# Optimization experiments

Hardware: AMD Instinct MI355X
Metric: run time of the kernel (lower is better)

The kernel has to match this reference:

```python
import jax, jax.numpy as jnp
import numpy as np

B, S, NC_CAND = 64, 200, 16
V, NCAT, D, NH, L = 100000, 1000, 256, 8, 2
EU, TKU = 4, 2   # user-block MoE uses EfficientMoELayer defaults
EI, TKI = 8, 2   # item MoE uses config num_experts/top_k
NE_CFG = 8       # load_balance_loss uniform always uses config.num_experts
HID = 2 * D

FLOAT_NAMES = ['item_emb', 'cat_emb', 'ub_in_w', 'ub_in_b', 'ub_out_w', 'ub_out_b',
               'ub_n1_s', 'ub_n1_b', 'ub_n2_s', 'ub_n2_b', 'ub_gate_w', 'ub_gate_b',
               'ub_e_w1', 'ub_e_b1', 'ub_e_w2', 'ub_e_b2', 'un_s', 'un_b',
               'im_gate_w', 'im_gate_b', 'im_e_w1', 'im_e_b1', 'im_e_w2', 'im_e_b2',
               'in_s', 'in_b', 'ca_in_w', 'ca_in_b', 'ca_out_w', 'ca_out_b',
               'fm_w1', 'fm_b1', 'fm_w2', 'fm_b2']


def _ln(x, s, b):
    m = jnp.mean(x, axis=-1, keepdims=True)
    v = jnp.mean((x - m) ** 2, axis=-1, keepdims=True)
    return (x - m) * jax.lax.rsqrt(v + 1e-5) * s + b


def _rope(x):
    # NOTE: faithful to the source's (unconventional) RoPE: x*cos + roll(x,-1)*sin
    s, d = x.shape[1], x.shape[2]
    inv = 1.0 / (10000.0 ** (jnp.arange(0, d, 2, dtype=jnp.float32) / d))
    f = jnp.arange(s, dtype=jnp.float32)[:, None] * inv[None, :]
    emb = jnp.concatenate([f, f], axis=-1)                      # [S, D]
    return x * jnp.cos(emb)[None] + jnp.roll(x, -1, axis=-1) * jnp.sin(emb)[None]


def _self_attn(x, wi, bi, wo, bo):
    b, s, d = x.shape
    hd = d // NH
    q, k, v = jnp.split(x @ wi.T + bi, 3, axis=-1)
    q = q.reshape(b, s, NH, hd)
    k = k.reshape(b, s, NH, hd)
    v = v.reshape(b, s, NH, hd)
    att = jax.nn.softmax(jnp.einsum('bqhd,bkhd->bhqk', q, k) * (hd ** -0.5), axis=-1)
    o = jnp.einsum('bhqk,bkhd->bqhd', att, v).reshape(b, s, d)
    return o @ wo.T + bo


def _moe(xf, gw, gb, w1, b1, w2, b2, top_k):
    # dense-expert compute + sparse top-k combine (same math as masked scatter loop)
    logits = xf @ gw.T + gb                                     # [T, E]
    w = jax.nn.softmax(logits.astype(jnp.float32), axis=-1)
    tw, ti = jax.lax.top_k(w, top_k)
    tw = tw / jnp.sum(tw, axis=-1, keepdims=True)
    e = gw.shape[0]
    cw = jnp.sum(jax.nn.one_hot(ti, e, dtype=tw.dtype) * tw[..., None], axis=1)  # [T, E]
    h = jax.nn.gelu(jnp.einsum('td,ehd->teh', xf, w1) + b1[None], approximate=False)
    y = jnp.einsum('teh,edh->ted', h, w2) + b2[None]
    return jnp.einsum('te,ted->td', cw.astype(xf.dtype), y), logits


def _forward(history_seq, candidate_ids, category_ids, p):
    x = _rope(p['item_emb'][history_seq])                       # [B, S, D]
    routers = []
    for l in range(L):
        a = _self_attn(x, p['ub_in_w'][l], p['ub_in_b'][l], p['ub_out_w'][l], p['ub_out_b'][l])
        x = _ln(x + a, p['ub_n1_s'][l], p['ub_n1_b'][l])
        mo, r = _moe(x.reshape(-1, D), p['ub_gate_w'][l], p['ub_gate_b'][l],
                     p['ub_e_w1'][l], p['ub_e_b1'][l], p['ub_e_w2'][l], p['ub_e_b2'][l], TKU)
        routers.append(r)
        x = _ln(x + mo.reshape(x.shape), p['ub_n2_s'][l], p['ub_n2_b'][l])
    hist = _ln(x, p['un_s'], p['un_b'])                          # [B, S, D]

    ie = p['item_emb'][candidate_ids] + p['cat_emb'][category_ids]  # [B, Nc, D]
    mo_i, r_i = _moe(ie.reshape(-1, D), p['im_gate_w'], p['im_gate_b'],
                     p['im_e_w1'], p['im_e_b1'], p['im_e_w2'], p['im_e_b2'], TKI)
    item = _ln(mo_i.reshape(ie.shape), p['in_s'], p['in_b'])     # [B, Nc, D]

    # cross attention: candidates as length-1 queries over history (no [B*Nc,S,D] expand)
    hd = D // NH
    wq, wk, wv = jnp.split(p['ca_in_w'], 3, axis=0)
    bq, bk, bv = jnp.split(p['ca_in_b'], 3, axis=0)
    q = (item @ wq.T + bq).reshape(B, NC_CAND, NH, hd)
    k = (hist @ wk.T + bk).reshape(B, S, NH, hd)
    v = (hist @ wv.T + bv).reshape(B, S, NH, hd)
    att = jax.nn.softmax(jnp.einsum('bnhd,bshd->bnhs', q, k) * (hd ** -0.5), axis=-1)
    o = jnp.einsum('bnhs,bshd->bnhd', att, v).reshape(B, NC_CAND, D)
    taw = o @ p['ca_out_w'].T + p['ca_out_b']                    # [B, Nc, D]

    fused = jnp.concatenate([taw, item], axis=-1)                # [B, Nc, 2D]
    h = jax.nn.gelu(fused @ p['fm_w1'].T + p['fm_b1'], approximate=False)
    logits = (h @ p['fm_w2'].T + p['fm_b2'])[..., 0]             # [B, Nc]

    aux = jnp.float32(0.0)
    for r in routers + [r_i]:
        avg = jnp.mean(jax.nn.softmax(r, axis=-1), axis=0)
        aux = aux + jnp.mean((avg - 1.0 / NE_CFG) ** 2)
    return logits, aux


def setup_inputs() -> dict:
    key = jax.random.key(0)
    ks = iter(jax.random.split(key, 64))

    def nrm(shape, scale=0.02):
        return jax.random.normal(next(ks), shape, jnp.float32) * scale

    inp = {
        'history_seq': jax.random.randint(next(ks), (B, S), 0, V),
        'candidate_ids': jax.random.randint(next(ks), (B, NC_CAND), 0, V),
        'category_ids': jax.random.randint(next(ks), (B, NC_CAND), 0, NCAT),
        'item_emb': nrm((V, D)), 'cat_emb': nrm((NCAT, D)),
        'ub_in_w': nrm((L, 3 * D, D)), 'ub_in_b': jnp.zeros((L, 3 * D), jnp.float32),
        'ub_out_w': nrm((L, D, D)), 'ub_out_b': jnp.zeros((L, D), jnp.float32),
        'ub_n1_s': jnp.ones((L, D), jnp.float32), 'ub_n1_b': jnp.zeros((L, D), jnp.float32),
        'ub_n2_s': jnp.ones((L, D), jnp.float32), 'ub_n2_b': jnp.zeros((L, D), jnp.float32),
        'ub_gate_w': nrm((L, EU, D)), 'ub_gate_b': jnp.zeros((L, EU), jnp.float32),
        'ub_e_w1': nrm((L, EU, HID, D)), 'ub_e_b1': jnp.zeros((L, EU, HID), jnp.float32),
        'ub_e_w2': nrm((L, EU, D, HID)), 'ub_e_b2': jnp.zeros((L, EU, D), jnp.float32),
        'un_s': jnp.ones((D,), jnp.float32), 'un_b': jnp.zeros((D,), jnp.float32),
        'im_gate_w': nrm((EI, D)), 'im_gate_b': jnp.zeros((EI,), jnp.float32),
        'im_e_w1': nrm((EI, HID, D)), 'im_e_b1': jnp.zeros((EI, HID), jnp.float32),
        'im_e_w2': nrm((EI, D, HID)), 'im_e_b2': jnp.zeros((EI, D), jnp.float32),
        'in_s': jnp.ones((D,), jnp.float32), 'in_b': jnp.zeros((D,), jnp.float32),
        'ca_in_w': nrm((3 * D, D)), 'ca_in_b': jnp.zeros((3 * D,), jnp.float32),
        'ca_out_w': nrm((D, D)), 'ca_out_b': jnp.zeros((D,), jnp.float32),
        'fm_w1': nrm((D, 2 * D)), 'fm_b1': jnp.zeros((D,), jnp.float32),
        'fm_w2': nrm((1, D)), 'fm_b2': jnp.zeros((1,), jnp.float32),
    }
    return inp


def reference(history_seq, candidate_ids, category_ids, item_emb, cat_emb,
              ub_in_w, ub_in_b, ub_out_w, ub_out_b, ub_n1_s, ub_n1_b, ub_n2_s, ub_n2_b,
              ub_gate_w, ub_gate_b, ub_e_w1, ub_e_b1, ub_e_w2, ub_e_b2, un_s, un_b,
              im_gate_w, im_gate_b, im_e_w1, im_e_b1, im_e_w2, im_e_b2, in_s, in_b,
              ca_in_w, ca_in_b, ca_out_w, ca_out_b, fm_w1, fm_b1, fm_w2, fm_b2):
    lv = locals()
    p = {k: lv[k] for k in FLOAT_NAMES}
    return _forward(history_seq, candidate_ids, category_ids, p)
```

## Files before the change

kernel.cpp:

```cpp
#include <hip/hip_runtime.h>
#include <cstddef>
#include <cstdint>

#define T_U   12800
#define T_I   1024
#define CAP_U 26112
#define CAP_I 3072

using short8 = __attribute__((ext_vector_type(8))) short;
using f32x4  = __attribute__((ext_vector_type(4))) float;

__device__ __forceinline__ float gelu_f(float x) {
  return 0.5f * x * (1.0f + erff(x * 0.7071067811865476f));
}

__device__ __forceinline__ void bf16_split(float x, unsigned short& h, unsigned short& l) {
  unsigned int u = __float_as_uint(x);
  unsigned short hs = (unsigned short)((u + 0x7FFFu + ((u >> 16) & 1u)) >> 16);
  float hf = __uint_as_float(((unsigned int)hs) << 16);
  float r = x - hf;
  unsigned int u2 = __float_as_uint(r);
  unsigned short ls = (unsigned short)((u2 + 0x7FFFu + ((u2 >> 16) & 1u)) >> 16);
  h = hs; l = ls;
}

__device__ __forceinline__ void split8v(float4 a, float4 b, short8& h, short8& l) {
  unsigned short hh, ll;
  bf16_split(a.x, hh, ll); h[0] = (short)hh; l[0] = (short)ll;
  bf16_split(a.y, hh, ll); h[1] = (short)hh; l[1] = (short)ll;
  bf16_split(a.z, hh, ll); h[2] = (short)hh; l[2] = (short)ll;
  bf16_split(a.w, hh, ll); h[3] = (short)hh; l[3] = (short)ll;
  bf16_split(b.x, hh, ll); h[4] = (short)hh; l[4] = (short)ll;
  bf16_split(b.y, hh, ll); h[5] = (short)hh; l[5] = (short)ll;
  bf16_split(b.z, hh, ll); h[6] = (short)hh; l[6] = (short)ll;
  bf16_split(b.w, hh, ll); h[7] = (short)hh; l[7] = (short)ll;
}

__device__ __forceinline__ void psplit8(float4 a, float4 b, short8& h, short8& l) {
  unsigned int u; float x;
#define PS_(VAL, i)                                     \
  u = __float_as_uint(VAL);                             \
  h[i] = (short)(u >> 16);                              \
  x = (VAL) - __uint_as_float(u & 0xFFFF0000u);         \
  l[i] = (short)(__float_as_uint(x) >> 16);
  PS_(a.x, 0) PS_(a.y, 1) PS_(a.z, 2) PS_(a.w, 3)
  PS_(b.x, 4) PS_(b.y, 5) PS_(b.z, 6) PS_(b.w, 7)
#undef PS_
}

#define FMA16(a, b, acc)                                                        \
  acc[0][0] += a.x * b.x; acc[0][1] += a.x * b.y; acc[0][2] += a.x * b.z; acc[0][3] += a.x * b.w; \
  acc[1][0] += a.y * b.x; acc[1][1] += a.y * b.y; acc[1][2] += a.y * b.z; acc[1][3] += a.y * b.w; \
  acc[2][0] += a.z * b.x; acc[2][1] += a.z * b.y; acc[2][2] += a.z * b.z; acc[2][3] += a.z * b.w; \
  acc[3][0] += a.w * b.x; acc[3][1] += a.w * b.y; acc[3][2] += a.w * b.z; acc[3][3] += a.w * b.w;

__global__ void k_sentinel(float* out) { out[0] = 1.0e9f; }

__global__ __launch_bounds__(256) void k_cvt(
    const float* __restrict__ in, unsigned short* __restrict__ hi,
    unsigned short* __restrict__ lo, int n4)
{
  int i = blockIdx.x * 256 + threadIdx.x;
  if (i >= n4) return;
  float4 v = ((const float4*)in)[i];
  ushort4 h, l;
  bf16_split(v.x, h.x, l.x);
  bf16_split(v.y, h.y, l.y);
  bf16_split(v.z, h.z, l.z);
  bf16_split(v.w, h.w, l.w);
  ((ushort4*)hi)[i] = h;
  ((ushort4*)lo)[i] = l;
}

__global__ __launch_bounds__(256) void k_embed_rope(
    const int* __restrict__ hist, const float* __restrict__ emb, float* __restrict__ X)
{
  int t = blockIdx.x;
  int s = t % 200;
  int d = threadIdx.x;
  const float* row = emb + (size_t)hist[t] * 256;
  float x0 = row[d];
  float x1 = row[(d + 1) & 255];
  int fi = d & 127;
  float inv = expf(-9.210340371976184f * ((float)fi * (1.0f / 128.0f)));
  float ang = (float)s * inv;
  X[(size_t)t * 256 + d] = x0 * cosf(ang) + x1 * sinf(ang);
}

__global__ __launch_bounds__(256) void k_item_embed(
    const int* __restrict__ cand, const int* __restrict__ catid,
    const float* __restrict__ item_emb, const float* __restrict__ cat_emb,
    float* __restrict__ IE)
{
  int t = blockIdx.x, d = threadIdx.x;
  IE[(size_t)t * 256 + d] =
      item_emb[(size_t)cand[t] * 256 + d] + cat_emb[(size_t)catid[t] * 256 + d];
}

__global__ __launch_bounds__(256) void k_gemm(
    const float* __restrict__ A, const float* __restrict__ Wm,
    const float* __restrict__ bias, float* __restrict__ C,
    int M, int N, int K, int act)
{
  __shared__ float As[16][68];
  __shared__ float Ws[16][68];
  int tid = threadIdx.x;
  int row0 = blockIdx.y << 6;
  int col0 = blockIdx.x << 6;
  int lr = tid >> 2, lk = (tid & 3) << 2;
  int tx = tid & 15, ty = tid >> 4;
  const float* Aload = A + (size_t)(row0 + lr) * K + lk;
  const float* Wload = Wm + (size_t)(col0 + lr) * K + lk;
  float acc[4][4] = {};
  for (int k0 = 0; k0 < K; k0 += 16) {
    float4 av = *(const float4*)(Aload + k0);
    float4 wv = *(const float4*)(Wload + k0);
    As[lk][lr] = av.x; As[lk + 1][lr] = av.y; As[lk + 2][lr] = av.z; As[lk + 3][lr] = av.w;
    Ws[lk][lr] = wv.x; Ws[lk + 1][lr] = wv.y; Ws[lk + 2][lr] = wv.z; Ws[lk + 3][lr] = wv.w;
    __syncthreads();
#pragma unroll
    for (int k = 0; k < 16; ++k) {
      float4 a = *(const float4*)&As[k][ty << 2];
      float4 b = *(const float4*)&Ws[k][tx << 2];
      FMA16(a, b, acc);
    }
    __syncthreads();
  }
#pragma unroll
  for (int i = 0; i < 4; ++i) {
// ... 29 lines not shown
    bp += (size_t)e * N;
  }
  int col0 = blockIdx.x << 7;
  __shared__ unsigned short sAh[128 * 40];
  __shared__ unsigned short sAl[128 * 40];
  __shared__ unsigned short sWh[128 * 40];
  __shared__ unsigned short sWl[128 * 40];
  int tid = threadIdx.x;
  int R = tid >> 2, kc = tid & 3;
  const unsigned short *pA0h, *pA0l, *pA1h, *pA1l;
  bool z0 = false, z1 = false;
  if (tok) {
    int t0 = tok[row0 + R];
    int t1 = tok[row0 + R + 64];
    if (t0 < 0) { z0 = true; pA0h = pA0l = Ahi; }
    else { pA0h = Ahi + (size_t)t0 * K; pA0l = Alo + (size_t)t0 * K; }
    if (t1 < 0) { z1 = true; pA1h = pA1l = Ahi; }
    else { pA1h = Ahi + (size_t)t1 * K; pA1l = Alo + (size_t)t1 * K; }
  } else {
    pA0h = Ahi + (size_t)(row0 + R) * K;      pA0l = Alo + (size_t)(row0 + R) * K;
    pA1h = Ahi + (size_t)(row0 + R + 64) * K; pA1l = Alo + (size_t)(row0 + R + 64) * K;
  }
  const unsigned short* pW0h = Wh + (size_t)(col0 + R) * K;
  const unsigned short* pW0l = Wl + (size_t)(col0 + R) * K;
  const unsigned short* pW1h = Wh + (size_t)(col0 + R + 64) * K;
  const unsigned short* pW1l = Wl + (size_t)(col0 + R + 64) * K;

  int wv = tid >> 6, lane = tid & 63;
  int wr = (wv & 1) << 6, wc = (wv >> 1) << 6;
  int fr = lane & 15, kg = (lane >> 4) << 3;

  f32x4 acc[4][4] = {};
  const uint4 zero4 = make_uint4(0u, 0u, 0u, 0u);
  for (int k0 = 0; k0 < K; k0 += 32) {
    int go = k0 + kc * 8;
    uint4 a0h = z0 ? zero4 : *(const uint4*)(pA0h + go);
    uint4 a0l = z0 ? zero4 : *(const uint4*)(pA0l + go);
    uint4 a1h = z1 ? zero4 : *(const uint4*)(pA1h + go);
    uint4 a1l = z1 ? zero4 : *(const uint4*)(pA1l + go);
    uint4 w0h = *(const uint4*)(pW0h + go);
    uint4 w0l = *(const uint4*)(pW0l + go);
    uint4 w1h = *(const uint4*)(pW1h + go);
    uint4 w1l = *(const uint4*)(pW1l + go);
    __syncthreads();
    int so = R * 40 + kc * 8;
    *(uint4*)(sAh + so) = a0h;          *(uint4*)(sAl + so) = a0l;
    *(uint4*)(sAh + so + 64 * 40) = a1h; *(uint4*)(sAl + so + 64 * 40) = a1l;
    *(uint4*)(sWh + so) = w0h;          *(uint4*)(sWl + so) = w0l;
    *(uint4*)(sWh + so + 64 * 40) = w1h; *(uint4*)(sWl + so + 64 * 40) = w1l;
    __syncthreads();
    short8 ah[4], al[4], bh[4], bl[4];
#pragma unroll
    for (int mi = 0; mi < 4; ++mi) {
      int a = (wr + mi * 16 + fr) * 40 + kg;
      ah[mi] = *(const short8*)(sAh + a);
      al[mi] = *(const short8*)(sAl + a);
    }
#pragma unroll
    for (int ni = 0; ni < 4; ++ni) {
      int a = (wc + ni * 16 + fr) * 40 + kg;
      bh[ni] = *(const short8*)(sWh + a);
      bl[ni] = *(const short8*)(sWl + a);
    }
#pragma unroll
    for (int mi = 0; mi < 4; ++mi) {
#pragma unroll
      for (int ni = 0; ni < 4; ++ni) {
        acc[mi][ni] = __builtin_amdgcn_mfma_f32_16x16x32_bf16(ah[mi], bh[ni], acc[mi][ni], 0, 0, 0);
        acc[mi][ni] = __builtin_amdgcn_mfma_f32_16x16x32_bf16(ah[mi], bl[ni], acc[mi][ni], 0, 0, 0);
        acc[mi][ni] = __builtin_amdgcn_mfma_f32_16x16x32_bf16(al[mi], bh[ni], acc[mi][ni], 0, 0, 0);
      }
    }
  }
  int fr4 = (lane >> 4) << 2;
#pragma unroll
  for (int ni = 0; ni < 4; ++ni) {
    int gcol = col0 + wc + ni * 16 + fr;
    float bv = bp[gcol];
#pragma unroll
    for (int mi = 0; mi < 4; ++mi) {
#pragma unroll
      for (int r = 0; r < 4; ++r) {
        float v = acc[mi][ni][r] + bv;
        if (act) v = gelu_f(v);
        size_t grow = (size_t)(row0 + wr + mi * 16 + fr4 + r);
        if (OutF) {
          OutF[grow * ldOut + gcol] = v;
        } else {
          unsigned short h, l;
          bf16_split(v, h, l);
          OutHi[grow * ldOut + gcol] = h;
          OutLo[grow * ldOut + gcol] = l;
        }
      }
    }
  }
}

__global__ __launch_bounds__(256, 2) void k_mfmm_y(
    const unsigned short* __restrict__ Ahi, const unsigned short* __restrict__ Alo,
    const int* __restrict__ offs, int E,
    const unsigned short* __restrict__ Whi, const unsigned short* __restrict__ Wlo,
    const float* __restrict__ bias, float* __restrict__ OutF, int K)
{
  const int N = 256;
  int row0 = blockIdx.y << 6;
  if (row0 >= offs[E]) return;
  int e = E - 1;
  while (e > 0 && offs[e] > row0) --e;
  const unsigned short* Wh = Whi + (size_t)e * N * K;
  const unsigned short* Wl = Wlo + (size_t)e * N * K;
  const float* bp = bias + (size_t)e * N;
  __shared__ unsigned short sAh[64 * 40];
  __shared__ unsigned short sAl[64 * 40];
  __shared__ unsigned short sWh[256 * 40];
  __shared__ unsigned short sWl[256 * 40];
  int tid = threadIdx.x;
  int R = tid >> 2, kc = tid & 3;
  const unsigned short* pAh = Ahi + (size_t)(row0 + R) * K;
  const unsigned short* pAl = Alo + (size_t)(row0 + R) * K;
  const unsigned short* pWh = Wh + (size_t)R * K;
  const unsigned short* pWl = Wl + (size_t)R * K;

  int wv = tid >> 6, lane = tid & 63;
  int wc = wv << 6;
  int fr = lane & 15, kg = (lane >> 4) << 3;

  f32x4 acc[4][4] = {};
  for (int k0 = 0; k0 < K; k0 += 32) {
    int go = k0 + kc * 8;
    uint4 a0h = *(const uint4*)(pAh + go);
    uint4 a0l = *(const uint4*)(pAl + go);
    uint4 w0h = *(const uint4*)(pWh + go);
    uint4 w0l = *(const uint4*)(pWl + go);
    uint4 w1h = *(const uint4*)(pWh + (size_t)64 * K + go);
    uint4 w1l = *(const uint4*)(pWl + (size_t)64 * K + go);
    uint4 w2h = *(const uint4*)(pWh + (size_t)128 * K + go);
    uint4 w2l = *(const uint4*)(pWl + (size_t)128 * K + go);
    uint4 w3h = *(const uint4*)(pWh + (size_t)192 * K + go);
    uint4 w3l = *(const uint4*)(pWl + (size_t)192 * K + go);
    __syncthreads();
    int so = R * 40 + kc * 8;
    *(uint4*)(sAh + so) = a0h;            *(uint4*)(sAl + so) = a0l;
    *(uint4*)(sWh + so) = w0h;            *(uint4*)(sWl + so) = w0l;
    *(uint4*)(sWh + so + 64 * 40) = w1h;  *(uint4*)(sWl + so + 64 * 40) = w1l;
    *(uint4*)(sWh + so + 128 * 40) = w2h; *(uint4*)(sWl + so + 128 * 40) = w2l;
    *(uint4*)(sWh + so + 192 * 40) = w3h; *(uint4*)(sWl + so + 192 * 40) = w3l;
    __syncthreads();
    short8 ah[4], al[4], bh[4], bl[4];
#pragma unroll
    for (int mi = 0; mi < 4; ++mi) {
      int a = (mi * 16 + fr) * 40 + kg;
      ah[mi] = *(const short8*)(sAh + a);
      al[mi] = *(const short8*)(sAl + a);
    }
#pragma unroll
    for (int ni = 0; ni < 4; ++ni) {
      int a = (wc + ni * 16 + fr) * 40 + kg;
      bh[ni] = *(const short8*)(sWh + a);
      bl[ni] = *(const short8*)(sWl + a);
    }
#pragma unroll
    for (int mi = 0; mi < 4; ++mi) {
#pragma unroll
      for (int ni = 0; ni < 4; ++ni) {
        acc[mi][ni] = __builtin_amdgcn_mfma_f32_16x16x32_bf16(ah[mi], bh[ni], acc[mi][ni], 0, 0, 0);
        acc[mi][ni] = __builtin_amdgcn_mfma_f32_16x16x32_bf16(ah[mi], bl[ni], acc[mi][ni], 0, 0, 0);
        acc[mi][ni] = __builtin_amdgcn_mfma_f32_16x16x32_bf16(al[mi], bh[ni], acc[mi][ni], 0, 0, 0);
      }
    }
  }
  int fr4 = (lane >> 4) << 2;
#pragma unroll
  for (int ni = 0; ni < 4; ++ni) {
    int gcol = wc + ni * 16 + fr;
    float bv = bp[gcol];
#pragma unroll
    for (int mi = 0; mi < 4; ++mi) {
#pragma unroll
      for (int r = 0; r < 4; ++r) {
        size_t grow = (size_t)(row0 + mi * 16 + fr4 + r);
        OutF[grow * 256 + gcol] = acc[mi][ni][r] + bv;
      }
    }
  }
}

#define ATT_LDK 40
#define ATT_LDV 216
#define ATT_LDP 212
__global__ __launch_bounds__(256) void k_attn_mfma(
    const float* __restrict__ qkv, float* __restrict__ ao)
{
  __shared__ unsigned short sKh[208 * ATT_LDK];
  __shared__ unsigned short sKl[208 * ATT_LDK];
  __shared__ unsigned short sVh[32 * ATT_LDV];
  __shared__ unsigned short sVl[32 * ATT_LDV];
  __shared__ float sP[4 * 16 * ATT_LDP];
  int bh = blockIdx.x;
  int b = bh >> 3, h = bh & 7;
  const float* base = qkv + (size_t)b * 200 * 768 + h * 32;
  int tid = threadIdx.x;
  for (int i = tid; i < 1600; i += 256) {
    int s = i >> 3, d4 = (i & 7) << 2;
    float4 kv = *(const float4*)(base + (size_t)s * 768 + 256 + d4);
    float4 vv = *(const float4*)(base + (size_t)s * 768 + 512 + d4);
    ushort4 kh, kl;
    bf16_split(kv.x, kh.x, kl.x);
    bf16_split(kv.y, kh.y, kl.y);
    bf16_split(kv.z, kh.z, kl.z);
    bf16_split(kv.w, kh.w, kl.w);
    *(ushort4*)(sKh + s * ATT_LDK + d4) = kh;
    *(ushort4*)(sKl + s * ATT_LDK + d4) = kl;
    unsigned short vh, vl;
    bf16_split(vv.x, vh, vl); sVh[(d4 + 0) * ATT_LDV + s] = vh; sVl[(d4 + 0) * ATT_LDV + s] = vl;
    bf16_split(vv.y, vh, vl); sVh[(d4 + 1) * ATT_LDV + s] = vh; sVl[(d4 + 1) * ATT_LDV + s] = vl;
    bf16_split(vv.z, vh, vl); sVh[(d4 + 2) * ATT_LDV + s] = vh; sVl[(d4 + 2) * ATT_LDV + s] = vl;
    bf16_split(vv.w, vh, vl); sVh[(d4 + 3) * ATT_LDV + s] = vh; sVl[(d4 + 3) * ATT_LDV + s] = vl;
  }
  for (int i = tid; i < 8 * ATT_LDK; i += 256) {
    sKh[200 * ATT_LDK + i] = 0; sKl[200 * ATT_LDK + i] = 0;
  }
  for (int i = tid; i < 32 * 16; i += 256) {
    int d = i >> 4, c = 200 + (i & 15);
    sVh[d * ATT_LDV + c] = 0; sVl[d * ATT_LDV + c] = 0;
// ... 66 lines not shown
    for (int ks = 0; ks < 7; ++ks) {
      short8 pah = {}, pal = {}, v0h = {}, v0l = {}, v1h = {}, v1l = {};
      if (ks < 6 || g < 2) {
        const float* pr = Pf + fr * ATT_LDP + ks * 32 + g * 8;
        float4 p0 = *(const float4*)pr;
        float4 p1 = *(const float4*)(pr + 4);
        psplit8(p0, p1, pah, pal);
        int ko = ks * 32 + g * 8;
        v0h = *(const short8*)(sVh + fr * ATT_LDV + ko);
        v0l = *(const short8*)(sVl + fr * ATT_LDV + ko);
        v1h = *(const short8*)(sVh + (16 + fr) * ATT_LDV + ko);
        v1l = *(const short8*)(sVl + (16 + fr) * ATT_LDV + ko);
      }
      if (ks & 1) {
        o01 = __builtin_amdgcn_mfma_f32_16x16x32_bf16(pah, v0h, o01, 0, 0, 0);
        o01 = __builtin_amdgcn_mfma_f32_16x16x32_bf16(pah, v0l, o01, 0, 0, 0);
        o01 = __builtin_amdgcn_mfma_f32_16x16x32_bf16(pal, v0h, o01, 0, 0, 0);
        o11 = __builtin_amdgcn_mfma_f32_16x16x32_bf16(pah, v1h, o11, 0, 0, 0);
        o11 = __builtin_amdgcn_mfma_f32_16x16x32_bf16(pah, v1l, o11, 0, 0, 0);
        o11 = __builtin_amdgcn_mfma_f32_16x16x32_bf16(pal, v1h, o11, 0, 0, 0);
      } else {
        o00 = __builtin_amdgcn_mfma_f32_16x16x32_bf16(pah, v0h, o00, 0, 0, 0);
        o00 = __builtin_amdgcn_mfma_f32_16x16x32_bf16(pah, v0l, o00, 0, 0, 0);
        o00 = __builtin_amdgcn_mfma_f32_16x16x32_bf16(pal, v0h, o00, 0, 0, 0);
        o10 = __builtin_amdgcn_mfma_f32_16x16x32_bf16(pah, v1h, o10, 0, 0, 0);
        o10 = __builtin_amdgcn_mfma_f32_16x16x32_bf16(pah, v1l, o10, 0, 0, 0);
        o10 = __builtin_amdgcn_mfma_f32_16x16x32_bf16(pal, v1h, o10, 0, 0, 0);
      }
    }
#pragma unroll
    for (int r = 0; r < 4; ++r) {
      int qr = qbase + g * 4 + r;
      if (qr < 200) {
        float* op = ao + (size_t)(b * 200 + qr) * 256 + h * 32;
        op[fr]      = (o00[r] + o01[r]) * sum[r];
        op[16 + fr] = (o10[r] + o11[r]) * sum[r];
      }
    }
  }
}

__global__ __launch_bounds__(256) void k_xattn(
    const float* __restrict__ Q, const float* __restrict__ Kb,
    const float* __restrict__ Vb, float* __restrict__ O)
{
  __shared__ float4 Ks[200 * 9];
  __shared__ float4 Vs[200 * 9];
  __shared__ float4 Qs[16 * 9];
  __shared__ float  Sc[16 * 209];
  __shared__ float  red[16 * 16];
  __shared__ float  mq_s[16], linv_s[16];
  int bh = blockIdx.x;
  int b = bh >> 3, h = bh & 7;
  int tid = threadIdx.x;
  for (int i = tid; i < 1600; i += 256) {
    int s = i >> 3, d = i & 7;
    Ks[s * 9 + d] = *(const float4*)(Kb + (size_t)(b * 200 + s) * 256 + h * 32 + d * 4);
    Vs[s * 9 + d] = *(const float4*)(Vb + (size_t)(b * 200 + s) * 256 + h * 32 + d * 4);
  }
  if (tid < 128) {
    int q = tid >> 3, d = tid & 7;
    Qs[q * 9 + d] = *(const float4*)(Q + (size_t)(b * 16 + q) * 256 + h * 32 + d * 4);
  }
  __syncthreads();
  const float scale = 0.17677669529663687f;
  int q = tid >> 4, si = tid & 15;
  float4 qr[8];
#pragma unroll
  for (int d = 0; d < 8; ++d) qr[d] = Qs[q * 9 + d];
// ... 30 lines not shown
    int s = si + 16 * j;
    if (s < 200) {
      float e = expf(sc[j] - mq);
      Sc[q * 209 + s] = e;
      ls += e;
    }
  }
  red[q * 16 + si] = ls;
  __syncthreads();
  if (tid < 16) {
    float s = 0.f;
#pragma unroll
    for (int k = 0; k < 16; ++k) s += red[tid * 16 + k];
    linv_s[tid] = 1.f / s;
  }
  __syncthreads();
  if (tid < 128) {
    int qq = tid >> 3, dd = tid & 7;
    float4 o = make_float4(0.f, 0.f, 0.f, 0.f);
    const float* prow = &Sc[qq * 209];
    for (int s = 0; s < 200; ++s) {
      float p = prow[s];
      float4 vv = Vs[s * 9 + dd];
      o.x += p * vv.x; o.y += p * vv.y; o.z += p * vv.z; o.w += p * vv.w;
    }
    float inv = linv_s[qq];
    o.x *= inv; o.y *= inv; o.z *= inv; o.w *= inv;
    *(float4*)(O + (size_t)(b * 16 + qq) * 256 + h * 32 + dd * 4) = o;
  }
}

__global__ __launch_bounds__(256) void k_ln(
    const float* __restrict__ Xin, const float* __restrict__ R,
    const float* __restrict__ sc, const float* __restrict__ bi, float* __restrict__ Y)
{
  int t = blockIdx.x, d = threadIdx.x;
  size_t idx = (size_t)t * 256 + d;
  float v = Xin[idx];
  if (R) v += R[idx];
  __shared__ float red[8];
  int lane = d & 63, wid = d >> 6;
  float s = v;
#pragma unroll
  for (int off = 32; off > 0; off >>= 1) s += __shfl_xor(s, off, 64);
  if (lane == 0) red[wid] = s;
  __syncthreads();
  float mean = (red[0] + red[1] + red[2] + red[3]) * 0.00390625f;
  float dv = v - mean;
  float s2 = dv * dv;
#pragma unroll
  for (int off = 32; off > 0; off >>= 1) s2 += __shfl_xor(s2, off, 64);
  if (lane == 0) red[4 + wid] = s2;
  __syncthreads();
  float var = (red[4] + red[5] + red[6] + red[7]) * 0.00390625f;
  Y[idx] = dv * (1.0f / sqrtf(var + 1e-5f)) * sc[d] + bi[d];
}

__global__ __launch_bounds__(256) void k_ln_comb(
    const float* __restrict__ Xin, const float* __restrict__ Yb, int ldY,
    const int* __restrict__ slotmap, const float* __restrict__ tw,
    const float* __restrict__ sc, const float* __restrict__ bi, float* __restrict__ Y)
{
  int t = blockIdx.x, d = threadIdx.x;
  size_t idx = (size_t)t * 256 + d;
  int s0 = slotmap[2 * t], s1 = slotmap[2 * t + 1];
  float w0 = tw[2 * t], w1 = tw[2 * t + 1];
  float v = w0 * Yb[(size_t)s0 * ldY + d] + w1 * Yb[(size_t)s1 * ldY + d];
  if (Xin) v += Xin[idx];
  __shared__ float red[8];
  int lane = d & 63, wid = d >> 6;
  float s = v;
#pragma unroll
  for (int off = 32; off > 0; off >>= 1) s += __shfl_xor(s, off, 64);
  if (lane == 0) red[wid] = s;
  __syncthreads();
  float mean = (red[0] + red[1] + red[2] + red[3]) * 0.00390625f;
  float dv = v - mean;
  float s2 = dv * dv;
#pragma unroll
  for (int off = 32; off > 0; off >>= 1) s2 += __shfl_xor(s2, off, 64);
  if (lane == 0) red[4 + wid] = s2;
  __syncthreads();
  float var = (red[4] + red[5] + red[6] + red[7]) * 0.00390625f;
  Y[idx] = dv * (1.0f / sqrtf(var + 1e-5f)) * sc[d] + bi[d];
}

template <int E>
__global__ __launch_bounds__(256) void k_router(
    const float* __restrict__ X, int T,
    const float* __restrict__ gw, const float* __restrict__ gb,
    float* __restrict__ probs, int* __restrict__ ti, float* __restrict__ tw)
{
  int lane = threadIdx.x & 63, wid = threadIdx.x >> 6;
  int t = blockIdx.x * 4 + wid;
  if (t >= T) return;
  float4 x4 = *(const float4*)(X + (size_t)t * 256 + lane * 4);
  float p[E];
#pragma unroll
  for (int e = 0; e < E; ++e) {
    float4 g = *(const float4*)(gw + (size_t)e * 256 + lane * 4);
    float s = x4.x * g.x + x4.y * g.y + x4.z * g.z + x4.w * g.w;
#pragma unroll
    for (int off = 32; off > 0; off >>= 1) s += __shfl_xor(s, off, 64);
    p[e] = s + gb[e];
  }
  float m = p[0];
#pragma unroll
  for (int e = 1; e < E; ++e) m = fmaxf(m, p[e]);
  float sum = 0.f;
#pragma unroll
  for (int e = 0; e < E; ++e) { p[e] = expf(p[e] - m); sum += p[e]; }
  float inv = 1.f / sum;
#pragma unroll
  for (int e = 0; e < E; ++e) p[e] *= inv;
  if (lane < E) probs[(size_t)t * E + lane] = p[lane];
  if (lane == 0) {
    float v1 = p[0]; int i1 = 0;
// ... 186 lines not shown
  const float* ca_out_w = (const float*)d_in[31];
  const float* ca_out_b = (const float*)d_in[32];
  const float* fm_w1    = (const float*)d_in[33];
  const float* fm_b1    = (const float*)d_in[34];
  const float* fm_w2    = (const float*)d_in[35];
  const float* fm_b2    = (const float*)d_in[36];
  float* out = (float*)d_out;

  float* W = (float*)d_ws;
  size_t o = 0;
  auto alloc = [&](size_t n) { size_t r = o; o += (n + 63) & ~(size_t)63; return r; };
  const size_t oX    = alloc((size_t)T_U * 256);
  const size_t oQKV  = alloc((size_t)T_U * 768);
  const size_t oAO   = alloc((size_t)T_U * 256);
  const size_t oEXT  = alloc(300000);
  const size_t oTMP  = alloc((size_t)T_U * 256);
  const size_t oP0   = alloc((size_t)T_U * 4);
  const size_t oP1   = alloc((size_t)T_U * 4);
  const size_t oPI   = alloc((size_t)T_I * 8);
  const size_t oTW   = alloc((size_t)T_U * 2);
  const size_t oSM   = alloc((size_t)T_U * 2);
  const size_t oTI   = alloc((size_t)T_U * 2);
  const size_t oTOK  = alloc(CAP_U);
  const size_t oCNT  = alloc(64);
  const size_t oIE   = alloc((size_t)T_I * 256);
  const size_t oITEM = alloc((size_t)T_I * 256);
  const size_t oQB   = alloc((size_t)T_I * 256);
  const size_t oOB   = alloc((size_t)T_I * 256);
  const size_t oTAW  = alloc((size_t)T_I * 256);
  const size_t oFUS  = alloc((size_t)T_I * 512);
  const size_t oFH   = alloc((size_t)T_I * 256);
  const size_t oWB   = alloc(4915200);
  const size_t oCVT  = alloc((size_t)T_U * 256);
  (void)oEXT;
  if (ws_size < o * sizeof(float)) {
    k_sentinel<<<1, 1, 0, stream>>>(out);
    return;
  }

  float* X    = W + oX;
  float* QKV  = W + oQKV;
  float* AO   = W + oAO;
  float* TMP  = W + oTMP;
  float* P0   = W + oP0;
  float* P1   = W + oP1;
  float* PI   = W + oPI;
  float* TWb  = W + oTW;
  int*   SLOT = (int*)(W + oSM);
  int*   TIb  = (int*)(W + oTI);
  int*   TOKb = (int*)(W + oTOK);
  int*   CNT  = (int*)(W + oCNT);
  int*   CNT2 = CNT;
  int*   OFFS = CNT + 8;
  float* IE   = W + oIE;
  float* ITEM = W + oITEM;
  float* QB   = W + oQB;
  float* OB   = W + oOB;
  float* TAW  = W + oTAW;
  float* FUS  = W + oFUS;
  float* FH   = W + oFH;
  float* Kbuf = QKV;
  float* Vbuf = QKV + (size_t)T_U * 256;

  unsigned short* WH = (unsigned short*)(W + oWB);
  unsigned short* WL = WH + 4915200;
  const size_t off_in = 0, off_out = 393216, off_ew1 = 524288, off_ew2 = 1572864,
               off_iw1 = 2621440, off_iw2 = 3670016, off_ca = 4718592;
  unsigned short* CVH = (unsigned short*)(W + oCVT);
  unsigned short* CVL = CVH + (size_t)T_U * 256;
  unsigned short* Hhi = (unsigned short*)(W + oQKV);
  unsigned short* Hlo = Hhi + (size_t)CAP_U * 512;
  float* Yu = (float*)Hlo;
  unsigned short* iHhi = (unsigned short*)(W + oQKV);
  unsigned short* iHlo = iHhi + (size_t)CAP_I * 512;
  float* Yi = (float*)iHlo;

  k_cvt<<<384, 256, 0, stream>>>(ub_in_w,  WH + off_in,  WL + off_in,  393216 / 4);
  k_cvt<<<128, 256, 0, stream>>>(ub_out_w, WH + off_out, WL + off_out, 131072 / 4);
  k_cvt<<<1024, 256, 0, stream>>>(ub_e_w1, WH + off_ew1, WL + off_ew1, 1048576 / 4);
  k_cvt<<<1024, 256, 0, stream>>>(ub_e_w2, WH + off_ew2, WL + off_ew2, 1048576 / 4);
  k_cvt<<<1024, 256, 0, stream>>>(im_e_w1, WH + off_iw1, WL + off_iw1, 1048576 / 4);
  k_cvt<<<1024, 256, 0, stream>>>(im_e_w2, WH + off_iw2, WL + off_iw2, 1048576 / 4);
  k_cvt<<<192, 256, 0, stream>>>(ca_in_w,  WH + off_ca,  WL + off_ca,  196608 / 4);

  k_embed_rope<<<T_U, 256, 0, stream>>>(history, item_emb, X);

  for (int l = 0; l < 2; ++l) {
    k_cvt<<<3200, 256, 0, stream>>>(X, CVH, CVL, T_U * 256 / 4);
    k_mfmm<<<dim3(6, 100), 256, 0, stream>>>(CVH, CVL, nullptr, nullptr, 0,
        WH + off_in + (size_t)l * 196608, WL + off_in + (size_t)l * 196608,
        ub_in_b + l * 768, QKV, nullptr, nullptr, 768, 256, 768, 0);
    k_attn_mfma<<<512, 256, 0, stream>>>(QKV, AO);
    k_cvt<<<3200, 256, 0, stream>>>(AO, CVH, CVL, T_U * 256 / 4);
    k_mfmm<<<dim3(2, 100), 256, 0, stream>>>(CVH, CVL, nullptr, nullptr, 0,
        WH + off_out + (size_t)l * 65536, WL + off_out + (size_t)l * 65536,
        ub_out_b + l * 256, TMP, nullptr, nullptr, 256, 256, 256, 0);
    k_ln<<<T_U, 256, 0, stream>>>(X, TMP, ub_n1_s + l * 256, ub_n1_b + l * 256, X);
    k_router<4><<<T_U / 4, 256, 0, stream>>>(X, T_U, ub_gate_w + (size_t)l * 4 * 256,
        ub_gate_b + l * 4, (l == 0) ? P0 : P1, TIb, TWb);
    k_count_scan<4><<<1, 256, 0, stream>>>(TIb, T_U, OFFS, CNT2, TOKb);
    k_fill<<<T_U / 256, 256, 0, stream>>>(TIb, T_U, OFFS, CNT2, TOKb, SLOT);
    k_cvt<<<3200, 256, 0, stream>>>(X, CVH, CVL, T_U * 256 / 4);
    k_mfmm<<<dim3(4, CAP_U / 128), 256, 0, stream>>>(CVH, CVL, TOKb, OFFS, 4,
        WH + off_ew1 + (size_t)l * 524288, WL + off_ew1 + (size_t)l * 524288,
        ub_e_b1 + (size_t)l * 2048, nullptr, Hhi, Hlo, 512, 256, 512, 1);
    k_mfmm_y<<<dim3(1, CAP_U / 64), 256, 0, stream>>>(Hhi, Hlo, OFFS, 4,
        WH + off_ew2 + (size_t)l * 524288, WL + off_ew2 + (size_t)l * 524288,
        ub_e_b2 + (size_t)l * 1024, Yu, 512);
    k_ln_comb<<<T_U, 256, 0, stream>>>(X, Yu, 256, SLOT, TWb,
        ub_n2_s + l * 256, ub_n2_b + l * 256, X);
  }

  k_ln<<<T_U, 256, 0, stream>>>(X, nullptr, un_s, un_b, X);

  k_item_embed<<<T_I, 256, 0, stream>>>(cand, catid, item_emb, cat_emb, IE);
  k_router<8><<<T_I / 4, 256, 0, stream>>>(IE, T_I, im_gate_w, im_gate_b, PI, TIb, TWb);
  k_count_scan<8><<<1, 256, 0, stream>>>(TIb, T_I, OFFS, CNT2, TOKb);
  k_fill<<<T_I / 256, 256, 0, stream>>>(TIb, T_I, OFFS, CNT2, TOKb, SLOT);
  k_cvt<<<256, 256, 0, stream>>>(IE, CVH, CVL, T_I * 256 / 4);
  k_mfmm<<<dim3(4, CAP_I / 128), 256, 0, stream>>>(CVH, CVL, TOKb, OFFS, 8,
      WH + off_iw1, WL + off_iw1, im_e_b1, nullptr, iHhi, iHlo, 512, 256, 512, 1);
  k_mfmm_y<<<dim3(1, CAP_I / 64), 256, 0, stream>>>(iHhi, iHlo, OFFS, 8,
      WH + off_iw2, WL + off_iw2, im_e_b2, Yi, 512);
  k_ln_comb<<<T_I, 256, 0, stream>>>(nullptr, Yi, 256, SLOT, TWb, in_s, in_b, ITEM);

  k_gemm<<<dim3(4, 16), 256, 0, stream>>>(ITEM, ca_in_w, ca_in_b, QB, T_I, 256, 256, 0);
  k_cvt<<<3200, 256, 0, stream>>>(X, CVH, CVL, T_U * 256 / 4);
  k_mfmm<<<dim3(2, 100), 256, 0, stream>>>(CVH, CVL, nullptr, nullptr, 0,
      WH + off_ca + 65536, WL + off_ca + 65536, ca_in_b + 256,
      Kbuf, nullptr, nullptr, 256, 256, 256, 0);
  k_mfmm<<<dim3(2, 100), 256, 0, stream>>>(CVH, CVL, nullptr, nullptr, 0,
      WH + off_ca + 131072, WL + off_ca + 131072, ca_in_b + 512,
      Vbuf, nullptr, nullptr, 256, 256, 256, 0);
  k_xattn<<<512, 256, 0, stream>>>(QB, Kbuf, Vbuf, OB);
  k_gemm<<<dim3(4, 16), 256, 0, stream>>>(OB, ca_out_w, ca_out_b, TAW, T_I, 256, 256, 0);

  k_concat<<<(T_I * 512) / 256, 256, 0, stream>>>(TAW, ITEM, FUS, T_I * 512);
  k_gemm<<<dim3(4, 16), 256, 0, stream>>>(FUS, fm_w1, fm_b1, FH, T_I, 256, 512, 1);
  k_final<<<T_I / 4, 256, 0, stream>>>(FH, fm_w2, fm_b2, out, T_I);

  k_aux<<<1, 256, 0, stream>>>(P0, P1, PI, out + 1024);
}
```

Measured before the change: 995.4 us.

## Fuse bf16 hi/lo split into producers and double-buffer MFMA GEMM loads

```diff
diff --git a/kernel.cpp b/kernel.cpp
--- a/kernel.cpp
+++ b/kernel.cpp
@@ -48,6 +48,12 @@
 #undef PS_
 }
 
+__device__ __forceinline__ void wg_barrier() {
+  asm volatile("" ::: "memory");
+  __builtin_amdgcn_s_barrier();
+  asm volatile("" ::: "memory");
+}
+
 #define FMA16(a, b, acc)                                                        \
   acc[0][0] += a.x * b.x; acc[0][1] += a.x * b.y; acc[0][2] += a.x * b.z; acc[0][3] += a.x * b.w; \
   acc[1][0] += a.y * b.x; acc[1][1] += a.y * b.y; acc[1][2] += a.y * b.z; acc[1][3] += a.y * b.w; \
@@ -73,7 +79,8 @@
 }
 
 __global__ __launch_bounds__(256) void k_embed_rope(
-    const int* __restrict__ hist, const float* __restrict__ emb, float* __restrict__ X)
+    const int* __restrict__ hist, const float* __restrict__ emb, float* __restrict__ X,
+    unsigned short* __restrict__ XH, unsigned short* __restrict__ XL)
 {
   int t = blockIdx.x;
   int s = t % 200;
@@ -84,17 +91,26 @@
   int fi = d & 127;
   float inv = expf(-9.210340371976184f * ((float)fi * (1.0f / 128.0f)));
   float ang = (float)s * inv;
-  X[(size_t)t * 256 + d] = x0 * cosf(ang) + x1 * sinf(ang);
+  float v = x0 * cosf(ang) + x1 * sinf(ang);
+  size_t idx = (size_t)t * 256 + d;
+  X[idx] = v;
+  unsigned short hh, ll;
+  bf16_split(v, hh, ll);
+  XH[idx] = hh; XL[idx] = ll;
 }
 
 __global__ __launch_bounds__(256) void k_item_embed(
     const int* __restrict__ cand, const int* __restrict__ catid,
     const float* __restrict__ item_emb, const float* __restrict__ cat_emb,
-    float* __restrict__ IE)
+    float* __restrict__ IE, unsigned short* __restrict__ IH, unsigned short* __restrict__ IL)
 {
   int t = blockIdx.x, d = threadIdx.x;
-  IE[(size_t)t * 256 + d] =
-      item_emb[(size_t)cand[t] * 256 + d] + cat_emb[(size_t)catid[t] * 256 + d];
+  float v = item_emb[(size_t)cand[t] * 256 + d] + cat_emb[(size_t)catid[t] * 256 + d];
+  size_t idx = (size_t)t * 256 + d;
+  IE[idx] = v;
+  unsigned short hh, ll;
+  bf16_split(v, hh, ll);
+  IH[idx] = hh; IL[idx] = ll;
 }
 
 __global__ __launch_bounds__(256) void k_gemm(
@@ -190,23 +206,27 @@
 
   f32x4 acc[4][4] = {};
   const uint4 zero4 = make_uint4(0u, 0u, 0u, 0u);
-  for (int k0 = 0; k0 < K; k0 += 32) {
+  uint4 rA[8], rB[8];
+  int so = R * 40 + kc * 8;
+
+  auto LOADK = [&](uint4* r, int k0) {
     int go = k0 + kc * 8;
-    uint4 a0h = z0 ? zero4 : *(const uint4*)(pA0h + go);
-    uint4 a0l = z0 ? zero4 : *(const uint4*)(pA0l + go);
-    uint4 a1h = z1 ? zero4 : *(const uint4*)(pA1h + go);
-    uint4 a1l = z1 ? zero4 : *(const uint4*)(pA1l + go);
-    uint4 w0h = *(const uint4*)(pW0h + go);
-    uint4 w0l = *(const uint4*)(pW0l + go);
-    uint4 w1h = *(const uint4*)(pW1h + go);
-    uint4 w1l = *(const uint4*)(pW1l + go);
-    __syncthreads();
-    int so = R * 40 + kc * 8;
-    *(uint4*)(sAh + so) = a0h;          *(uint4*)(sAl + so) = a0l;
-    *(uint4*)(sAh + so + 64 * 40) = a1h; *(uint4*)(sAl + so + 64 * 40) = a1l;
-    *(uint4*)(sWh + so) = w0h;          *(uint4*)(sWl + so) = w0l;
-    *(uint4*)(sWh + so + 64 * 40) = w1h; *(uint4*)(sWl + so + 64 * 40) = w1l;
-    __syncthreads();
+    r[0] = z0 ? zero4 : *(const uint4*)(pA0h + go);
+    r[1] = z0 ? zero4 : *(const uint4*)(pA0l + go);
+    r[2] = z1 ? zero4 : *(const uint4*)(pA1h + go);
+    r[3] = z1 ? zero4 : *(const uint4*)(pA1l + go);
+    r[4] = *(const uint4*)(pW0h + go);
+    r[5] = *(const uint4*)(pW0l + go);
+    r[6] = *(const uint4*)(pW1h + go);
+    r[7] = *(const uint4*)(pW1l + go);
+  };
+  auto STORE = [&](uint4* r) {
+    *(uint4*)(sAh + so) = r[0];           *(uint4*)(sAl + so) = r[1];
+    *(uint4*)(sAh + so + 64 * 40) = r[2]; *(uint4*)(sAl + so + 64 * 40) = r[3];
+    *(uint4*)(sWh + so) = r[4];           *(uint4*)(sWl + so) = r[5];
+    *(uint4*)(sWh + so + 64 * 40) = r[6]; *(uint4*)(sWl + so + 64 * 40) = r[7];
+  };
+  auto COMPUTE = [&]() {
     short8 ah[4], al[4], bh[4], bl[4];
 #pragma unroll
     for (int mi = 0; mi < 4; ++mi) {
@@ -229,6 +249,23 @@
         acc[mi][ni] = __builtin_amdgcn_mfma_f32_16x16x32_bf16(al[mi], bh[ni], acc[mi][ni], 0, 0, 0);
       }
     }
+  };
+
+  int steps = K >> 5;
+  LOADK(rA, 0);
+  for (int s = 0; s < steps; s += 2) {
+    wg_barrier();
+    STORE(rA);
+    if (s + 1 < steps) LOADK(rB, (s + 1) << 5);
+    asm volatile("s_waitcnt lgkmcnt(0)" ::: "memory");
+    wg_barrier();
+    COMPUTE();
+    wg_barrier();
+    STORE(rB);
+    if (s + 2 < steps) LOADK(rA, (s + 2) << 5);
+    asm volatile("s_waitcnt lgkmcnt(0)" ::: "memory");
+    wg_barrier();
+    COMPUTE();
   }
   int fr4 = (lane >> 4) << 2;
 #pragma unroll
@@ -285,26 +322,31 @@
   int fr = lane & 15, kg = (lane >> 4) << 3;
 
   f32x4 acc[4][4] = {};
-  for (int k0 = 0; k0 < K; k0 += 32) {
+  uint4 rA[12], rB[12];
+  int so = R * 40 + kc * 8;
+
+  auto LOADK = [&](uint4* r, int k0) {
     int go = k0 + kc * 8;
-    uint4 a0h = *(const uint4*)(pAh + go);
-    uint4 a0l = *(const uint4*)(pAl + go);
-    uint4 w0h = *(const uint4*)(pWh + go);
-    uint4 w0l = *(const uint4*)(pWl + go);
-    uint4 w1h = *(const uint4*)(pWh + (size_t)64 * K + go);
-    uint4 w1l = *(const uint4*)(pWl + (size_t)64 * K + go);
-    uint4 w2h = *(const uint4*)(pWh + (size_t)128 * K + go);
-    uint4 w2l = *(const uint4*)(pWl + (size_t)128 * K + go);
-    uint4 w3h = *(const uint4*)(pWh + (size_t)192 * K + go);
-    uint4 w3l = *(const uint4*)(pWl + (size_t)192 * K + go);
-    __syncthreads();
-    int so = R * 40 + kc * 8;
-    *(uint4*)(sAh + so) = a0h;            *(uint4*)(sAl + so) = a0l;
-    *(uint4*)(sWh + so) = w0h;            *(uint4*)(sWl + so) = w0l;
-    *(uint4*)(sWh + so + 64 * 40) = w1h;  *(uint4*)(sWl + so + 64 * 40) = w1l;
-    *(uint4*)(sWh + so + 128 * 40) = w2h; *(uint4*)(sWl + so + 128 * 40) = w2l;
-    *(uint4*)(sWh + so + 192 * 40) = w3h; *(uint4*)(sWl + so + 192 * 40) = w3l;
-    __syncthreads();
+    r[0]  = *(const uint4*)(pAh + go);
+    r[1]  = *(const uint4*)(pAl + go);
+    r[2]  = *(const uint4*)(pWh + go);
+    r[3]  = *(const uint4*)(pWl + go);
+    r[4]  = *(const uint4*)(pWh + (size_t)64 * K + go);
+    r[5]  = *(const uint4*)(pWl + (size_t)64 * K + go);
+    r[6]  = *(const uint4*)(pWh + (size_t)128 * K + go);
+    r[7]  = *(const uint4*)(pWl + (size_t)128 * K + go);
+    r[8]  = *(const uint4*)(pWh + (size_t)192 * K + go);
+    r[9]  = *(const uint4*)(pWl + (size_t)192 * K + go);
+    r[10] = r[0]; r[11] = r[1];
+  };
+  auto STORE = [&](uint4* r) {
+    *(uint4*)(sAh + so) = r[0];            *(uint4*)(sAl + so) = r[1];
+    *(uint4*)(sWh + so) = r[2];            *(uint4*)(sWl + so) = r[3];
+    *(uint4*)(sWh + so + 64 * 40) = r[4];  *(uint4*)(sWl + so + 64 * 40) = r[5];
+    *(uint4*)(sWh + so + 128 * 40) = r[6]; *(uint4*)(sWl + so + 128 * 40) = r[7];
+    *(uint4*)(sWh + so + 192 * 40) = r[8]; *(uint4*)(sWl + so + 192 * 40) = r[9];
+  };
+  auto COMPUTE = [&]() {
     short8 ah[4], al[4], bh[4], bl[4];
 #pragma unroll
     for (int mi = 0; mi < 4; ++mi) {
@@ -327,6 +369,23 @@
         acc[mi][ni] = __builtin_amdgcn_mfma_f32_16x16x32_bf16(al[mi], bh[ni], acc[mi][ni], 0, 0, 0);
       }
     }
+  };
+
+  int steps = K >> 5;
+  LOADK(rA, 0);
+  for (int s = 0; s < steps; s += 2) {
+    wg_barrier();
+    STORE(rA);
+    if (s + 1 < steps) LOADK(rB, (s + 1) << 5);
+    asm volatile("s_waitcnt lgkmcnt(0)" ::: "memory");
+    wg_barrier();
+    COMPUTE();
+    wg_barrier();
+    STORE(rB);
+    if (s + 2 < steps) LOADK(rA, (s + 2) << 5);
+    asm volatile("s_waitcnt lgkmcnt(0)" ::: "memory");
+    wg_barrier();
+    COMPUTE();
   }
   int fr4 = (lane >> 4) << 2;
 #pragma unroll
@@ -348,7 +407,8 @@
 #define ATT_LDV 216
 #define ATT_LDP 212
 __global__ __launch_bounds__(256) void k_attn_mfma(
-    const float* __restrict__ qkv, float* __restrict__ ao)
+    const float* __restrict__ qkv,
+    unsigned short* __restrict__ aoh, unsigned short* __restrict__ aol)
 {
   __shared__ unsigned short sKh[208 * ATT_LDK];
   __shared__ unsigned short sKl[208 * ATT_LDK];
@@ -481,9 +541,12 @@
     for (int r = 0; r < 4; ++r) {
       int qr = qbase + g * 4 + r;
       if (qr < 200) {
-        float* op = ao + (size_t)(b * 200 + qr) * 256 + h * 32;
-        op[fr]      = (o00[r] + o01[r]) * sum[r];
-        op[16 + fr] = (o10[r] + o11[r]) * sum[r];
+        size_t ob = (size_t)(b * 200 + qr) * 256 + h * 32;
+        unsigned short hh, ll;
+        bf16_split((o00[r] + o01[r]) * sum[r], hh, ll);
+        aoh[ob + fr] = hh;      aol[ob + fr] = ll;
+        bf16_split((o10[r] + o11[r]) * sum[r], hh, ll);
+        aoh[ob + 16 + fr] = hh; aol[ob + 16 + fr] = ll;
       }
     }
   }
@@ -580,7 +643,8 @@
 
 __global__ __launch_bounds__(256) void k_ln(
     const float* __restrict__ Xin, const float* __restrict__ R,
-    const float* __restrict__ sc, const float* __restrict__ bi, float* __restrict__ Y)
+    const float* __restrict__ sc, const float* __restrict__ bi, float* __restrict__ Y,
+    unsigned short* __restrict__ oh, unsigned short* __restrict__ ol)
 {
   int t = blockIdx.x, d = threadIdx.x;
   size_t idx = (size_t)t * 256 + d;
@@ -601,13 +665,20 @@
   if (lane == 0) red[4 + wid] = s2;
   __syncthreads();
   float var = (red[4] + red[5] + red[6] + red[7]) * 0.00390625f;
-  Y[idx] = dv * (1.0f / sqrtf(var + 1e-5f)) * sc[d] + bi[d];
+  float y = dv * (1.0f / sqrtf(var + 1e-5f)) * sc[d] + bi[d];
+  Y[idx] = y;
+  if (oh) {
+    unsigned short hh, ll;
+    bf16_split(y, hh, ll);
+    oh[idx] = hh; ol[idx] = ll;
+  }
 }
 
 __global__ __launch_bounds__(256) void k_ln_comb(
     const float* __restrict__ Xin, const float* __restrict__ Yb, int ldY,
     const int* __restrict__ slotmap, const float* __restrict__ tw,
-    const float* __restrict__ sc, const float* __restrict__ bi, float* __restrict__ Y)
+    const float* __restrict__ sc, const float* __restrict__ bi, float* __restrict__ Y,
+    unsigned short* __restrict__ oh, unsigned short* __restrict__ ol)
 {
   int t = blockIdx.x, d = threadIdx.x;
   size_t idx = (size_t)t * 256 + d;
@@ -630,7 +701,13 @@
   if (lane == 0) red[4 + wid] = s2;
   __syncthreads();
   float var = (red[4] + red[5] + red[6] + red[7]) * 0.00390625f;
-  Y[idx] = dv * (1.0f / sqrtf(var + 1e-5f)) * sc[d] + bi[d];
+  float y = dv * (1.0f / sqrtf(var + 1e-5f)) * sc[d] + bi[d];
+  Y[idx] = y;
+  if (oh) {
+    unsigned short hh, ll;
+    bf16_split(y, hh, ll);
+    oh[idx] = hh; ol[idx] = ll;
+  }
 }
 
 template <int E>
@@ -883,6 +960,7 @@
   const size_t oFH   = alloc((size_t)T_I * 256);
   const size_t oWB   = alloc(4915200);
   const size_t oCVT  = alloc((size_t)T_U * 256);
+  const size_t oCVI  = alloc((size_t)T_I * 256);
   (void)oEXT;
   if (ws_size < o * sizeof(float)) {
     k_sentinel<<<1, 1, 0, stream>>>(out);
@@ -912,6 +990,7 @@
   float* FH   = W + oFH;
   float* Kbuf = QKV;
   float* Vbuf = QKV + (size_t)T_U * 256;
+  (void)AO;
 
   unsigned short* WH = (unsigned short*)(W + oWB);
   unsigned short* WL = WH + 4915200;
@@ -919,6 +998,8 @@
                off_iw1 = 2621440, off_iw2 = 3670016, off_ca = 4718592;
   unsigned short* CVH = (unsigned short*)(W + oCVT);
   unsigned short* CVL = CVH + (size_t)T_U * 256;
+  unsigned short* CIH = (unsigned short*)(W + oCVI);
+  unsigned short* CIL = CIH + (size_t)T_I * 256;
   unsigned short* Hhi = (unsigned short*)(W + oQKV);
   unsigned short* Hlo = Hhi + (size_t)CAP_U * 512;
   float* Yu = (float*)Hlo;
@@ -934,24 +1015,21 @@
   k_cvt<<<1024, 256, 0, stream>>>(im_e_w2, WH + off_iw2, WL + off_iw2, 1048576 / 4);
   k_cvt<<<192, 256, 0, stream>>>(ca_in_w,  WH + off_ca,  WL + off_ca,  196608 / 4);
 
-  k_embed_rope<<<T_U, 256, 0, stream>>>(history, item_emb, X);
+  k_embed_rope<<<T_U, 256, 0, stream>>>(history, item_emb, X, CVH, CVL);
 
   for (int l = 0; l < 2; ++l) {
-    k_cvt<<<3200, 256, 0, stream>>>(X, CVH, CVL, T_U * 256 / 4);
     k_mfmm<<<dim3(6, 100), 256, 0, stream>>>(CVH, CVL, nullptr, nullptr, 0,
         WH + off_in + (size_t)l * 196608, WL + off_in + (size_t)l * 196608,
         ub_in_b + l * 768, QKV, nullptr, nullptr, 768, 256, 768, 0);
-    k_attn_mfma<<<512, 256, 0, stream>>>(QKV, AO);
-    k_cvt<<<3200, 256, 0, stream>>>(AO, CVH, CVL, T_U * 256 / 4);
+    k_attn_mfma<<<512, 256, 0, stream>>>(QKV, CVH, CVL);
     k_mfmm<<<dim3(2, 100), 256, 0, stream>>>(CVH, CVL, nullptr, nullptr, 0,
         WH + off_out + (size_t)l * 65536, WL + off_out + (size_t)l * 65536,
         ub_out_b + l * 256, TMP, nullptr, nullptr, 256, 256, 256, 0);
-    k_ln<<<T_U, 256, 0, stream>>>(X, TMP, ub_n1_s + l * 256, ub_n1_b + l * 256, X);
+    k_ln<<<T_U, 256, 0, stream>>>(X, TMP, ub_n1_s + l * 256, ub_n1_b + l * 256, X, CVH, CVL);
     k_router<4><<<T_U / 4, 256, 0, stream>>>(X, T_U, ub_gate_w + (size_t)l * 4 * 256,
         ub_gate_b + l * 4, (l == 0) ? P0 : P1, TIb, TWb);
     k_count_scan<4><<<1, 256, 0, stream>>>(TIb, T_U, OFFS, CNT2, TOKb);
     k_fill<<<T_U / 256, 256, 0, stream>>>(TIb, T_U, OFFS, CNT2, TOKb, SLOT);
-    k_cvt<<<3200, 256, 0, stream>>>(X, CVH, CVL, T_U * 256 / 4);
     k_mfmm<<<dim3(4, CAP_U / 128), 256, 0, stream>>>(CVH, CVL, TOKb, OFFS, 4,
         WH + off_ew1 + (size_t)l * 524288, WL + off_ew1 + (size_t)l * 524288,
         ub_e_b1 + (size_t)l * 2048, nullptr, Hhi, Hlo, 512, 256, 512, 1);
@@ -959,24 +1037,24 @@
         WH + off_ew2 + (size_t)l * 524288, WL + off_ew2 + (size_t)l * 524288,
         ub_e_b2 + (size_t)l * 1024, Yu, 512);
     k_ln_comb<<<T_U, 256, 0, stream>>>(X, Yu, 256, SLOT, TWb,
-        ub_n2_s + l * 256, ub_n2_b + l * 256, X);
-  }
-
-  k_ln<<<T_U, 256, 0, stream>>>(X, nullptr, un_s, un_b, X);
-
-  k_item_embed<<<T_I, 256, 0, stream>>>(cand, catid, item_emb, cat_emb, IE);
+        ub_n2_s + l * 256, ub_n2_b + l * 256, X,
+        (l == 0) ? CVH : nullptr, (l == 0) ? CVL : nullptr);
+  }
+
+  k_ln<<<T_U, 256, 0, stream>>>(X, nullptr, un_s, un_b, X, CVH, CVL);
+
+  k_item_embed<<<T_I, 256, 0, stream>>>(cand, catid, item_emb, cat_emb, IE, CIH, CIL);
   k_router<8><<<T_I / 4, 256, 0, stream>>>(IE, T_I, im_gate_w, im_gate_b, PI, TIb, TWb);
   k_count_scan<8><<<1, 256, 0, stream>>>(TIb, T_I, OFFS, CNT2, TOKb);
   k_fill<<<T_I / 256, 256, 0, stream>>>(TIb, T_I, OFFS, CNT2, TOKb, SLOT);
-  k_cvt<<<256, 256, 0, stream>>>(IE, CVH, CVL, T_I * 256 / 4);
-  k_mfmm<<<dim3(4, CAP_I / 128), 256, 0, stream>>>(CVH, CVL, TOKb, OFFS, 8,
+  k_mfmm<<<dim3(4, CAP_I / 128), 256, 0, stream>>>(CIH, CIL, TOKb, OFFS, 8,
       WH + off_iw1, WL + off_iw1, im_e_b1, nullptr, iHhi, iHlo, 512, 256, 512, 1);
   k_mfmm_y<<<dim3(1, CAP_I / 64), 256, 0, stream>>>(iHhi, iHlo, OFFS, 8,
       WH + off_iw2, WL + off_iw2, im_e_b2, Yi, 512);
-  k_ln_comb<<<T_I, 256, 0, stream>>>(nullptr, Yi, 256, SLOT, TWb, in_s, in_b, ITEM);
+  k_ln_comb<<<T_I, 256, 0, stream>>>(nullptr, Yi, 256, SLOT, TWb, in_s, in_b, ITEM,
+                                     nullptr, nullptr);
 
   k_gemm<<<dim3(4, 16), 256, 0, stream>>>(ITEM, ca_in_w, ca_in_b, QB, T_I, 256, 256, 0);
-  k_cvt<<<3200, 256, 0, stream>>>(X, CVH, CVL, T_U * 256 / 4);
   k_mfmm<<<dim3(2, 100), 256, 0, stream>>>(CVH, CVL, nullptr, nullptr, 0,
       WH + off_ca + 65536, WL + off_ca + 65536, ca_in_b + 256,
       Kbuf, nullptr, nullptr, 256, 256, 256, 0);
```

Measured after the change: 1.295 ms. +30.1%, slower.
